# Optimization experiments

Hardware: AMD Instinct MI355X
Metric: run time of the kernel (lower is better)

The kernel has to match this reference:

```python
import jax, jax.numpy as jnp
import numpy as np

GROUPS = 32
EPS = 1e-5


def setup_inputs() -> dict:
    key = jax.random.key(0)
    ks = jax.random.split(key, 4)
    B, C, H, W = 4, 256, 64, 64
    x = jax.random.normal(ks[0], (B, C, H, W), dtype=jnp.float32)
    gn_w = jnp.ones((C,), jnp.float32)
    gn_b = jnp.zeros((C,), jnp.float32)
    qkv_w = jax.random.normal(ks[1], (3 * C, C), dtype=jnp.float32) * (C ** -0.5)
    qkv_b = jnp.zeros((3 * C,), jnp.float32)
    proj_w = jax.random.normal(ks[2], (C, C), dtype=jnp.float32) * (C ** -0.5)
    proj_b = jnp.zeros((C,), jnp.float32)
    return {"x": x, "gn_w": gn_w, "gn_b": gn_b, "qkv_w": qkv_w,
            "qkv_b": qkv_b, "proj_w": proj_w, "proj_b": proj_b}


def _group_norm(x, w, b):
    B, C, H, W = x.shape
    xr = x.reshape(B, GROUPS, -1)                      # [B, G, (C/G)*H*W]
    mean = xr.mean(axis=-1, keepdims=True)
    var = xr.var(axis=-1, keepdims=True)               # biased, like torch
    h = ((xr - mean) * jax.lax.rsqrt(var + EPS)).reshape(B, C, H, W)
    return h * w[None, :, None, None] + b[None, :, None, None]


def reference(x, gn_w, gn_b, qkv_w, qkv_b, proj_w, proj_b):
    B, C, H, W = x.shape
    h = _group_norm(x, gn_w, gn_b)
    # 1x1 conv == channel GEMM
    qkv = jnp.einsum('oc,bchw->bohw', qkv_w, h) + qkv_b[None, :, None, None]
    qkv = qkv.reshape(B, 3, C, H * W)
    q, k, v = qkv[:, 0], qkv[:, 1], qkv[:, 2]          # [B, C, N]
    scale = C ** (-0.5)
    attn = jax.nn.softmax(jnp.einsum('bci,bcj->bij', q, k) * scale, axis=-1)
    out = jnp.einsum('bij,bcj->bci', attn, v).reshape(B, C, H, W)
    out = jnp.einsum('oc,bchw->bohw', proj_w, out) + proj_b[None, :, None, None]
    return x + out
```

## Files before the change

### kernel.cpp

```cpp
#include <hip/hip_runtime.h>
#include <hip/hip_bf16.h>
#include <math.h>

typedef __bf16 bf16;
typedef __bf16 bf16x8 __attribute__((ext_vector_type(8)));
typedef __bf16 bf16x4 __attribute__((ext_vector_type(4)));
typedef float f32x4 __attribute__((ext_vector_type(4)));
typedef float f32x16 __attribute__((ext_vector_type(16)));

#define MFMA16(a, b, c) __builtin_amdgcn_mfma_f32_16x16x32_bf16(a, b, c, 0, 0, 0)
#define MFMA32(a, b, c) __builtin_amdgcn_mfma_f32_32x32x16_bf16(a, b, c, 0, 0, 0)

#define SCALEK 0.09016844005555896f

typedef const __attribute__((address_space(1))) void* gas_t;
typedef __attribute__((address_space(3))) void* las_t;

__global__ __launch_bounds__(256) void wcvt_kernel(const float* __restrict__ qw,
                                                   bf16* __restrict__ qwb) {
  int t = blockIdx.x * 256 + threadIdx.x;
  float4 v = *(const float4*)(qw + (size_t)t * 4);
  bf16x4 o;
  o[0] = (bf16)v.x; o[1] = (bf16)v.y; o[2] = (bf16)v.z; o[3] = (bf16)v.w;
  *(bf16x4*)(qwb + (size_t)t * 4) = o;
}

__global__ __launch_bounds__(256) void gn_kernel(
    const float* __restrict__ x, const float* __restrict__ gw,
    const float* __restrict__ gb, bf16* __restrict__ h) {
  const int bg = blockIdx.x;
  const int b = bg >> 5, g = bg & 31;
  const size_t base = (size_t)(b * 256 + g * 8) * 4096;
  const float* xp = x + base;
  bf16* hp = h + base;
  const int tid = threadIdx.x;

  float s = 0.f, ss = 0.f;
  for (int i = tid * 4; i < 32768; i += 1024) {
    float4 v = *(const float4*)(xp + i);
    s += v.x + v.y + v.z + v.w;
    ss += v.x * v.x + v.y * v.y + v.z * v.z + v.w * v.w;
  }
#pragma unroll
  for (int off = 32; off; off >>= 1) {
    s += __shfl_down(s, off);
    ss += __shfl_down(ss, off);
  }
  __shared__ float red[8];
  if ((tid & 63) == 0) {
    red[(tid >> 6) * 2] = s;
    red[(tid >> 6) * 2 + 1] = ss;
  }
  __syncthreads();
  s = red[0] + red[2] + red[4] + red[6];
  ss = red[1] + red[3] + red[5] + red[7];
  const float mean = s * (1.f / 32768.f);
  const float var = ss * (1.f / 32768.f) - mean * mean;
  const float rstd = rsqrtf(var + 1e-5f);

  for (int i = tid * 4; i < 32768; i += 1024) {
    float4 v = *(const float4*)(xp + i);
    int c = g * 8 + (i >> 12);
    float a = gw[c] * rstd;
    float b2 = gb[c] - mean * a;
    bf16x4 o;
    o[0] = (bf16)(v.x * a + b2);
    o[1] = (bf16)(v.y * a + b2);
    o[2] = (bf16)(v.z * a + b2);
    o[3] = (bf16)(v.w * a + b2);
    *(bf16x4*)(hp + i) = o;
  }
}

__global__ __launch_bounds__(256) void qkv_gemm(
    const bf16* __restrict__ h, const bf16* __restrict__ wb,
    const float* __restrict__ bias, bf16* __restrict__ qt,
    bf16* __restrict__ kt, bf16* __restrict__ vcm) {
  const int b = blockIdx.z;
  const int o0 = blockIdx.y * 64;
  const int p0 = blockIdx.x * 64;
  __shared__ bf16 Alds[2][64][32];
  __shared__ bf16 Blds[2][64][56];
  const int tid = threadIdx.x;
  const int lane = tid & 63, wid = tid >> 6;
  const int lr = lane & 15, lg = lane >> 4;
  const int wm = wid >> 1, wn = wid & 1;
  const bf16* hb = h + (size_t)b * 256 * 4096;

  const int arow = tid >> 2, ac8 = (tid & 3) * 8;
  const int bcc = tid >> 3, bp8 = (tid & 7) * 8;

#define QKV_STAGE_A(K0, BUF)                                                  \
  __builtin_amdgcn_global_load_lds(                                           \
      (gas_t)(const void*)(wb + (size_t)(o0 + arow) * 256 + (K0) + ac8),      \
      (las_t)(void*)(&Alds[BUF][0][0] + tid * 8), 16, 0, 0);

  f32x4 acc[2][2] = {};

  QKV_STAGE_A(0, 0);
  {
    bf16x8 v = *(const bf16x8*)(hb + (size_t)bcc * 4096 + p0 + bp8);
#pragma unroll
    for (int e = 0; e < 8; ++e) Blds[0][bp8 + e][bcc] = v[e];
  }
  __syncthreads();

  for (int k = 0; k < 8; ++k) {
    const int cur = k & 1, nb = cur ^ 1;
    if (k < 7) {
      QKV_STAGE_A((k + 1) * 32, nb);
      bf16x8 v =
          *(const bf16x8*)(hb + (size_t)((k + 1) * 32 + bcc) * 4096 + p0 + bp8);
#pragma unroll
      for (int e = 0; e < 8; ++e) Blds[nb][bp8 + e][bcc] = v[e];
    }
    bf16x8 af[2], bfr[2];
#pragma unroll
    for (int mi = 0; mi < 2; ++mi)
      af[mi] = *(const bf16x8*)&Alds[cur][wm * 32 + mi * 16 + lr][lg * 8];
#pragma unroll
    for (int ni = 0; ni < 2; ++ni)
      bfr[ni] = *(const bf16x8*)&Blds[cur][wn * 32 + ni * 16 + lr][lg * 8];
#pragma unroll
    for (int mi = 0; mi < 2; ++mi)
#pragma unroll
      for (int ni = 0; ni < 2; ++ni)
        acc[mi][ni] = MFMA16(af[mi], bfr[ni], acc[mi][ni]);
    __syncthreads();
  }
#undef QKV_STAGE_A

#pragma unroll
  for (int mi = 0; mi < 2; ++mi) {
#pragma unroll
    for (int ni = 0; ni < 2; ++ni) {
#pragma unroll
      for (int r = 0; r < 4; ++r) {
        int o = o0 + wm * 32 + mi * 16 + lg * 4 + r;
        int p = p0 + wn * 32 + ni * 16 + lr;
        float val = acc[mi][ni][r] + bias[o];
        if (o < 256) {
          qt[((size_t)b * 4096 + p) * 256 + o] = (bf16)val;
        } else if (o < 512) {
          kt[((size_t)b * 4096 + p) * 256 + (o - 256)] = (bf16)(val * SCALEK);
        } else {
          vcm[((size_t)b * 256 + (o - 512)) * 4096 + p] = (bf16)val;
        }
      }
    }
  }
}

template <int S>
__global__ __launch_bounds__(512, 2) void flash_attn(
    const bf16* __restrict__ qt, const bf16* __restrict__ kt,
    const bf16* __restrict__ vcm, bf16* __restrict__ Opart,
    float* __restrict__ l_g) {
  constexpr int NCOMBO = 4 * S;
  constexpr int CSH = (S == 4) ? 4 : (S == 2) ? 3 : 2;
  constexpr int NIT = (4096 / S) / 32;
  const int bid = blockIdx.x;
  const int combo = bid & (NCOMBO - 1);
  const int qtile = bid >> CSH;
  const int b = combo & 3;
  const int split = combo >> 2;
  const int i0 = qtile * 256;
  const int jbase = split * (4096 / S);

  __shared__ bf16 Klds[2][32][256];
  __shared__ bf16 Vlds[2][256][32];
  const int tid = threadIdx.x;
  const int lane = tid & 63, w = tid >> 6;
  const int ln = lane & 31;
  const int hv = lane >> 5;
  const bf16* qb = qt + (size_t)b * 4096 * 256;
  const bf16* kb = kt + (size_t)b * 4096 * 256;
  const bf16* vb = vcm + (size_t)b * 256 * 4096;

  const int qrow = i0 + w * 32 + ln;
  bf16x8 qf[16];
#pragma unroll
  for (int ks = 0; ks < 16; ++ks)
    qf[ks] = *(const bf16x8*)(qb + (size_t)qrow * 256 + ks * 16 + hv * 8);

  int koff[2], voff[2];
#pragma unroll
  for (int it = 0; it < 2; ++it) {
    int chunk = tid + 512 * it;
    int krow = chunk >> 5;
    koff[it] = krow * 256 + ((((chunk & 31) ^ (krow & 7)) * 8));
    int vrow = chunk >> 2;
    voff[it] = vrow * 4096 + (((chunk & 3) ^ ((vrow >> 2) & 3)) * 8);
  }

#define STAGE_K(JT, BUF)                                                      \
  {                                                                           \
    const int j0s = jbase + (JT) * 32;                                        \
    _Pragma("unroll") for (int it = 0; it < 2; ++it) {                        \
      int chunk = tid + 512 * it;                                             \
      __builtin_amdgcn_global_load_lds(                                       \
          (gas_t)(const void*)(kb + (size_t)j0s * 256 + koff[it]),            \
          (las_t)(void*)(&Klds[BUF][0][0] + chunk * 8), 16, 0, 0);            \
    }                                                                         \
  }
#define STAGE_V(JT, BUF)                                                      \
  {                                                                           \
    const int j0s = jbase + (JT) * 32;                                        \
    _Pragma("unroll") for (int it = 0; it < 2; ++it) {                        \
      int chunk = tid + 512 * it;                                             \
      __builtin_amdgcn_global_load_lds(                                       \
          (gas_t)(const void*)(vb + (size_t)j0s + voff[it]),                  \
          (las_t)(void*)(&Vlds[BUF][0][0] + chunk * 8), 16, 0, 0);            \
    }                                                                         \
  }

  float llane = 0.f;
  f32x16 accO[8] = {};
  const int kswz = ln & 7;
  const int vswz = (ln >> 2) & 3;

  STAGE_K(0, 0);
  STAGE_V(0, 0);
  asm volatile("s_waitcnt vmcnt(0)" ::: "memory");
  __builtin_amdgcn_s_barrier();

  f32x16 a0 = {}, a1 = {};
#pragma unroll
  for (int ks = 0; ks < 8; ++ks) {
    bf16x8 kf0 = *(const bf16x8*)&Klds[0][ln][((2 * ks + hv) ^ kswz) * 8];
    bf16x8 kf1 =
        *(const bf16x8*)&Klds[0][ln][((2 * (ks + 8) + hv) ^ kswz) * 8];
    a0 = MFMA32(kf0, qf[ks], a0);
    a1 = MFMA32(kf1, qf[ks + 8], a1);
  }
  if (NIT > 1) STAGE_K(1, 1);

  for (int t = 0; t < NIT; ++t) {
    asm volatile("s_waitcnt vmcnt(0)" ::: "memory");
    __builtin_amdgcn_s_barrier();

    if (t + 1 < NIT) STAGE_V(t + 1, (t + 1) & 1);
    if (t + 2 < NIT) STAGE_K(t + 2, t & 1);

    float pv[16];
#pragma unroll
    for (int r = 0; r < 16; ++r) pv[r] = exp2f(a0[r] + a1[r]);
    llane += (((pv[0] + pv[1]) + (pv[2] + pv[3])) +
              ((pv[4] + pv[5]) + (pv[6] + pv[7]))) +
             (((pv[8] + pv[9]) + (pv[10] + pv[11])) +
              ((pv[12] + pv[13]) + (pv[14] + pv[15])));

    int pk[8];
#pragma unroll
    for (int q4 = 0; q4 < 8; ++q4)
      asm("v_cvt_pk_bf16_f32 %0, %1, %2"
          : "=v"(pk[q4])
          : "v"(pv[q4 * 2]), "v"(pv[q4 * 2 + 1]));
    bf16x8 pfrag[2];
#pragma unroll
    for (int s = 0; s < 2; ++s) {
      int xa = pk[s * 4 + 0], ya = pk[s * 4 + 2];
      int xb = pk[s * 4 + 1], yb = pk[s * 4 + 3];
      asm("v_permlane32_swap_b32 %0, %1" : "+v"(xa), "+v"(ya));
      asm("v_permlane32_swap_b32 %0, %1" : "+v"(xb), "+v"(yb));
      union { int i[4]; bf16x8 v; } u;
      u.i[0] = xa; u.i[1] = xb; u.i[2] = ya; u.i[3] = yb;
      pfrag[s] = u.v;
    }

    const bf16(*Kc)[256] = Klds[(t + 1) & 1];
    const bf16(*Vc)[32] = Vlds[t & 1];
    __builtin_amdgcn_s_setprio(1);
    if (t + 1 < NIT) {
      f32x16 n0 = {}, n1 = {};
#pragma unroll
      for (int u = 0; u < 8; ++u) {
        bf16x8 kf0 = *(const bf16x8*)&Kc[ln][((2 * u + hv) ^ kswz) * 8];
        n0 = MFMA32(kf0, qf[u], n0);
        bf16x8 kf1 =
            *(const bf16x8*)&Kc[ln][((2 * (u + 8) + hv) ^ kswz) * 8];
        n1 = MFMA32(kf1, qf[u + 8], n1);
        bf16x8 vf0 = *(const bf16x8*)&Vc[u * 32 + ln][((hv) ^ vswz) * 8];
        accO[u] = MFMA32(vf0, pfrag[0], accO[u]);
        bf16x8 vf1 = *(const bf16x8*)&Vc[u * 32 + ln][((2 + hv) ^ vswz) * 8];
        accO[u] = MFMA32(vf1, pfrag[1], accO[u]);
      }
      a0 = n0;
      a1 = n1;
    } else {
#pragma unroll
      for (int u = 0; u < 8; ++u) {
        bf16x8 vf0 = *(const bf16x8*)&Vc[u * 32 + ln][((hv) ^ vswz) * 8];
        accO[u] = MFMA32(vf0, pfrag[0], accO[u]);
        bf16x8 vf1 = *(const bf16x8*)&Vc[u * 32 + ln][((2 + hv) ^ vswz) * 8];
        accO[u] = MFMA32(vf1, pfrag[1], accO[u]);
      }
    }
    __builtin_amdgcn_s_setprio(0);
  }
#undef STAGE_K
#undef STAGE_V

  bf16* ob = Opart + ((size_t)(split * 4 + b) * 4096 + qrow) * 256;
#pragma unroll
  for (int cb = 0; cb < 8; ++cb) {
#pragma unroll
    for (int g = 0; g < 4; ++g) {
      int lo, hi;
      asm("v_cvt_pk_bf16_f32 %0, %1, %2"
          : "=v"(lo)
          : "v"(accO[cb][g * 4 + 0]), "v"(accO[cb][g * 4 + 1]));
      asm("v_cvt_pk_bf16_f32 %0, %1, %2"
          : "=v"(hi)
          : "v"(accO[cb][g * 4 + 2]), "v"(accO[cb][g * 4 + 3]));
      int2 val; val.x = lo; val.y = hi;
      *(int2*)(ob + cb * 32 + g * 8 + hv * 4) = val;
    }
  }
  {
    int xa = __float_as_int(llane);
    int ya = xa;
    asm("v_permlane32_swap_b32 %0, %1" : "+v"(xa), "+v"(ya));
    float ltot = __int_as_float(xa) + __int_as_float(ya);
    if (hv == 0)
      l_g[(size_t)(split * 4 + b) * 4096 + qrow] = ltot;
  }
}

template <int S>
__global__ __launch_bounds__(256) void proj_fused(
    const bf16* __restrict__ Opart, const float* __restrict__ l_g,
    const float* __restrict__ w, const float* __restrict__ bias,
    const float* __restrict__ x, float* __restrict__ out) {
  const int b = blockIdx.y;
  const int p0 = blockIdx.x * 64;
  __shared__ bf16 Wlds[256][32];
  __shared__ bf16 Blds[64][32];
  __shared__ float Linv[64];
  const int tid = threadIdx.x;
  const int lane = tid & 63, wid = tid >> 6;
  const int lr = lane & 15, lg = lane >> 4;

  if (tid < 64) {
    float L = 0.f;
#pragma unroll
    for (int s = 0; s < S; ++s)
      L += l_g[(size_t)(s * 4 + b) * 4096 + p0 + tid];
    Linv[tid] = 1.f / L;
  }
  __syncthreads();

  const int pr = tid >> 2, c8b = (tid & 3) * 8;
  const float invp = Linv[pr];

  float4 wreg[4][2];
  bf16x8 breg[S];

#define PROJ_READ(K0)                                                         \
  {                                                                           \
    _Pragma("unroll") for (int it = 0; it < 4; ++it) {                        \
      int chunk = tid + 256 * it;                                             \
      int row = chunk >> 2, c8 = (chunk & 3) * 8;                             \
      const float* src = w + (size_t)row * 256 + (K0) + c8;                   \
      wreg[it][0] = *(const float4*)src;                                      \
      wreg[it][1] = *(const float4*)(src + 4);                                \
    }                                                                         \
    _Pragma("unroll") for (int s = 0; s < S; ++s) breg[s] =                   \
        *(const bf16x8*)(Opart +                                              \
                         ((size_t)(s * 4 + b) * 4096 + p0 + pr) * 256 +       \
                         (K0) + c8b);                                         \
  }
#define PROJ_WRITE()                                                          \
  {                                                                           \
    _Pragma("unroll") for (int it = 0; it < 4; ++it) {                        \
      int chunk = tid + 256 * it;                                             \
      int row = chunk >> 2, c8 = (chunk & 3) * 8;                             \
      bf16x8 bv;                                                              \
      bv[0] = (bf16)wreg[it][0].x; bv[1] = (bf16)wreg[it][0].y;               \
      bv[2] = (bf16)wreg[it][0].z; bv[3] = (bf16)wreg[it][0].w;               \
      bv[4] = (bf16)wreg[it][1].x; bv[5] = (bf16)wreg[it][1].y;               \
      bv[6] = (bf16)wreg[it][1].z; bv[7] = (bf16)wreg[it][1].w;               \
      *(bf16x8*)&Wlds[row][c8] = bv;                                          \
    }                                                                         \
    {                                                                         \
      float a8[8] = {};                                                       \
      _Pragma("unroll") for (int s = 0; s < S; ++s) {                         \
        _Pragma("unroll") for (int e = 0; e < 8; ++e) a8[e] +=                \
            (float)breg[s][e];                                                \
      }                                                                       \
      bf16x8 bv;                                                              \
      _Pragma("unroll") for (int e = 0; e < 8; ++e) bv[e] =                   \
          (bf16)(a8[e] * invp);                                               \
      *(bf16x8*)&Blds[pr][c8b] = bv;                                          \
    }                                                                         \
  }

  f32x4 acc[4][4] = {};

  PROJ_READ(0);
  PROJ_WRITE();
  __syncthreads();

  for (int k = 0; k < 8; ++k) {
    if (k < 7) PROJ_READ((k + 1) * 32);

    bf16x8 af[4], bfr[4];
#pragma unroll
    for (int mi = 0; mi < 4; ++mi)
      af[mi] = *(const bf16x8*)&Wlds[wid * 64 + mi * 16 + lr][lg * 8];
#pragma unroll
    for (int ni = 0; ni < 4; ++ni)
      bfr[ni] = *(const bf16x8*)&Blds[ni * 16 + lr][lg * 8];
#pragma unroll
    for (int mi = 0; mi < 4; ++mi)
#pragma unroll
      for (int ni = 0; ni < 4; ++ni)
        acc[mi][ni] = MFMA16(af[mi], bfr[ni], acc[mi][ni]);

    __syncthreads();
    if (k < 7) {
      PROJ_WRITE();
      __syncthreads();
    }
  }
#undef PROJ_READ
#undef PROJ_WRITE

#pragma unroll
  for (int mi = 0; mi < 4; ++mi) {
#pragma unroll
    for (int ni = 0; ni < 4; ++ni) {
#pragma unroll
      for (int r = 0; r < 4; ++r) {
        int o = wid * 64 + mi * 16 + lg * 4 + r;
        int p = p0 + ni * 16 + lr;
        size_t idx = ((size_t)b * 256 + o) * 4096 + p;
        out[idx] = acc[mi][ni][r] + bias[o] + x[idx];
      }
    }
  }
}

extern "C" void kernel_launch(void* const* d_in, const int* in_sizes, int n_in,
                              void* d_out, int out_size, void* d_ws,
                              size_t ws_size, hipStream_t stream) {
  (void)in_sizes; (void)n_in; (void)out_size;
  const float* x = (const float*)d_in[0];
  const float* gn_w = (const float*)d_in[1];
  const float* gn_b = (const float*)d_in[2];
  const float* qkv_w = (const float*)d_in[3];
  const float* qkv_b = (const float*)d_in[4];
  const float* proj_w = (const float*)d_in[5];
  const float* proj_b = (const float*)d_in[6];
  float* out = (float*)d_out;

  const size_t MB = 1024ull * 1024ull;
  char* ws = (char*)d_ws;
  bf16* h = (bf16*)(ws);
  bf16* qt = (bf16*)(ws + 8 * MB);
  bf16* kt = (bf16*)(ws + 16 * MB);
  bf16* vcm = (bf16*)(ws + 24 * MB);

  int S;
  if (ws_size >= 32 * MB + 4 * 8 * MB + 4ull * 16384 * sizeof(float)) S = 4;
  else if (ws_size >= 32 * MB + 2 * 8 * MB + 2ull * 16384 * sizeof(float)) S = 2;
  else S = 1;

  bf16* Opart;
  float* l_g;
  bf16* qwb;
  if (S >= 2) {
    Opart = (bf16*)(ws + 32 * MB);
    l_g = (float*)(ws + 32 * MB + (size_t)S * 8 * MB);
    qwb = Opart;
  } else {
    Opart = h;
    l_g = (float*)(ws + 32 * MB);
    qwb = (bf16*)(ws + 32 * MB + 256 * 1024);
  }

  wcvt_kernel<<<192, 256, 0, stream>>>(qkv_w, qwb);
  gn_kernel<<<128, 256, 0, stream>>>(x, gn_w, gn_b, h);
  qkv_gemm<<<dim3(64, 12, 4), 256, 0, stream>>>(h, qwb, qkv_b, qt, kt, vcm);
  if (S == 4) {
    flash_attn<4><<<16 * 16, 512, 0, stream>>>(qt, kt, vcm, Opart, l_g);
    proj_fused<4><<<dim3(64, 4), 256, 0, stream>>>(Opart, l_g, proj_w, proj_b,
                                                   x, out);
  } else if (S == 2) {
    flash_attn<2><<<16 * 8, 512, 0, stream>>>(qt, kt, vcm, Opart, l_g);
    proj_fused<2><<<dim3(64, 4), 256, 0, stream>>>(Opart, l_g, proj_w, proj_b,
                                                   x, out);
  } else {
    flash_attn<1><<<16 * 4, 512, 0, stream>>>(qt, kt, vcm, Opart, l_g);
    proj_fused<1><<<dim3(64, 4), 256, 0, stream>>>(Opart, l_g, proj_w, proj_b,
                                                   x, out);
  }
}
```

Before: 171.1 us.

## Split group norm into per-channel stats and apply kernels for more parallelism

```diff
diff --git a/kernel.cpp b/kernel.cpp
--- a/kernel.cpp
+++ b/kernel.cpp
@@ -25,19 +25,16 @@
   *(bf16x4*)(qwb + (size_t)t * 4) = o;
 }
 
-__global__ __launch_bounds__(256) void gn_kernel(
-    const float* __restrict__ x, const float* __restrict__ gw,
-    const float* __restrict__ gb, bf16* __restrict__ h) {
-  const int bg = blockIdx.x;
-  const int b = bg >> 5, g = bg & 31;
-  const size_t base = (size_t)(b * 256 + g * 8) * 4096;
-  const float* xp = x + base;
-  bf16* hp = h + base;
+__global__ __launch_bounds__(256) void gn_stats(const float* __restrict__ x,
+                                                float* __restrict__ pstats) {
+  const int bid = blockIdx.x;
+  const float* xp = x + (size_t)bid * 4096;
   const int tid = threadIdx.x;
 
   float s = 0.f, ss = 0.f;
-  for (int i = tid * 4; i < 32768; i += 1024) {
-    float4 v = *(const float4*)(xp + i);
+#pragma unroll
+  for (int i = 0; i < 4; ++i) {
+    float4 v = *(const float4*)(xp + tid * 4 + i * 1024);
     s += v.x + v.y + v.z + v.w;
     ss += v.x * v.x + v.y * v.y + v.z * v.z + v.w * v.w;
   }
@@ -52,23 +49,44 @@
     red[(tid >> 6) * 2 + 1] = ss;
   }
   __syncthreads();
-  s = red[0] + red[2] + red[4] + red[6];
-  ss = red[1] + red[3] + red[5] + red[7];
+  if (tid == 0) {
+    pstats[bid * 2] = red[0] + red[2] + red[4] + red[6];
+    pstats[bid * 2 + 1] = red[1] + red[3] + red[5] + red[7];
+  }
+}
+
+__global__ __launch_bounds__(256) void gn_apply(
+    const float* __restrict__ x, const float* __restrict__ pstats,
+    const float* __restrict__ gw, const float* __restrict__ gb,
+    bf16* __restrict__ h) {
+  const int bid = blockIdx.x;
+  const int c = bid & 255;
+  const int gbase = bid & ~7;
+  const float* xp = x + (size_t)bid * 4096;
+  bf16* hp = h + (size_t)bid * 4096;
+  const int tid = threadIdx.x;
+
+  float s = 0.f, ss = 0.f;
+#pragma unroll
+  for (int i = 0; i < 8; ++i) {
+    s += pstats[(gbase + i) * 2];
+    ss += pstats[(gbase + i) * 2 + 1];
+  }
   const float mean = s * (1.f / 32768.f);
   const float var = ss * (1.f / 32768.f) - mean * mean;
   const float rstd = rsqrtf(var + 1e-5f);
-
-  for (int i = tid * 4; i < 32768; i += 1024) {
-    float4 v = *(const float4*)(xp + i);
-    int c = g * 8 + (i >> 12);
-    float a = gw[c] * rstd;
-    float b2 = gb[c] - mean * a;
+  const float a = gw[c] * rstd;
+  const float b2 = gb[c] - mean * a;
+
+#pragma unroll
+  for (int i = 0; i < 4; ++i) {
+    float4 v = *(const float4*)(xp + tid * 4 + i * 1024);
     bf16x4 o;
     o[0] = (bf16)(v.x * a + b2);
     o[1] = (bf16)(v.y * a + b2);
     o[2] = (bf16)(v.z * a + b2);
     o[3] = (bf16)(v.w * a + b2);
-    *(bf16x4*)(hp + i) = o;
+    *(bf16x4*)(hp + tid * 4 + i * 1024) = o;
   }
 }
 
@@ -462,9 +480,12 @@
   bf16* vcm = (bf16*)(ws + 24 * MB);
 
   int S;
-  if (ws_size >= 32 * MB + 4 * 8 * MB + 4ull * 16384 * sizeof(float)) S = 4;
-  else if (ws_size >= 32 * MB + 2 * 8 * MB + 2ull * 16384 * sizeof(float)) S = 2;
-  else S = 1;
+  if (ws_size >= 32 * MB + 4 * 8 * MB + 4ull * 16384 * sizeof(float) + 8192)
+    S = 4;
+  else if (ws_size >= 32 * MB + 2 * 8 * MB + 2ull * 16384 * sizeof(float) + 8192)
+    S = 2;
+  else
+    S = 1;
 
   bf16* Opart;
   float* l_g;
@@ -476,11 +497,13 @@
   } else {
     Opart = h;
     l_g = (float*)(ws + 32 * MB);
-    qwb = (bf16*)(ws + 32 * MB + 256 * 1024);
-  }
+    qwb = (bf16*)(ws + 32 * MB + 512 * 1024);
+  }
+  float* pstats = l_g + (size_t)S * 16384;
 
   wcvt_kernel<<<192, 256, 0, stream>>>(qkv_w, qwb);
-  gn_kernel<<<128, 256, 0, stream>>>(x, gn_w, gn_b, h);
+  gn_stats<<<1024, 256, 0, stream>>>(x, pstats);
+  gn_apply<<<1024, 256, 0, stream>>>(x, pstats, gn_w, gn_b, h);
   qkv_gemm<<<dim3(64, 12, 4), 256, 0, stream>>>(h, qwb, qkv_b, qt, kt, vcm);
   if (S == 4) {
     flash_attn<4><<<16 * 16, 512, 0, stream>>>(qt, kt, vcm, Opart, l_g);
```

Result: faster. 158.8 us (-7.2%).
